# Optimization experiments

Hardware: AMD Instinct MI355X
Metric: run time of the kernel (lower is better)

The kernel has to match this reference:

```python
import jax, jax.numpy as jnp
import numpy as np

B, N, DIM = 4, 2048, 1024
HEADS, DH = 16, 64
INNER = HEADS * DH
SCALE = 8.0
EPS = 1e-5


def setup_inputs() -> dict:
    key = jax.random.key(0)
    ks = jax.random.split(key, 8)
    x = jax.random.normal(ks[0], (B, N, DIM), dtype=jnp.float32)
    context_mask = jax.random.bernoulli(ks[1], 0.9, (B, N))
    gamma = jnp.ones((DIM,), dtype=jnp.float32)
    null_kv = jax.random.normal(ks[2], (2, HEADS, 1, DH), dtype=jnp.float32)
    Wq = jax.random.normal(ks[3], (DIM, INNER), dtype=jnp.float32) * 0.02
    Wkv = jax.random.normal(ks[4], (DIM, 2 * INNER), dtype=jnp.float32) * 0.02
    # q_scale init: scale / dim_head**-0.5 = 8 * sqrt(64) = 64
    q_scale = jnp.full((DH,), SCALE * (DH ** 0.5), dtype=jnp.float32)
    k_scale = jnp.ones((DH,), dtype=jnp.float32)
    Wout = jax.random.normal(ks[5], (INNER, DIM), dtype=jnp.float32) * 0.02
    return {"x": x, "context_mask": context_mask, "gamma": gamma,
            "null_kv": null_kv, "Wq": Wq, "Wkv": Wkv,
            "q_scale": q_scale, "k_scale": k_scale, "Wout": Wout}


def _l2norm(t):
    return t / jnp.sqrt(jnp.sum(t * t, axis=-1, keepdims=True) + 1e-12)


def reference(x, context_mask, gamma, null_kv, Wq, Wkv, q_scale, k_scale, Wout):
    b, n, _ = x.shape
    # LayerNorm (beta buffer is zeros)
    mu = jnp.mean(x, axis=-1, keepdims=True)
    var = jnp.mean((x - mu) ** 2, axis=-1, keepdims=True)
    xn = (x - mu) / jnp.sqrt(var + EPS) * gamma
    # projections
    q = (xn @ Wq).reshape(b, n, HEADS, DH)
    kv = xn @ Wkv
    k = kv[..., :INNER].reshape(b, n, HEADS, DH)
    v = kv[..., INNER:].reshape(b, n, HEADS, DH)
    # null kv token: [h,1,d] -> [b,1,h,d]
    nk = jnp.broadcast_to(null_kv[0].transpose(1, 0, 2)[None], (b, 1, HEADS, DH))
    nv = jnp.broadcast_to(null_kv[1].transpose(1, 0, 2)[None], (b, 1, HEADS, DH))
    k = jnp.concatenate([nk, k], axis=1)  # [b, n+1, h, d]
    v = jnp.concatenate([nv, v], axis=1)
    # cosine-sim attention with learned per-dim scales
    q = _l2norm(q) * q_scale
    k = _l2norm(k) * k_scale
    # bias from mask (padded True for null token)
    mask = jnp.pad(context_mask, ((0, 0), (1, 0)), constant_values=True)
    bias = jnp.where(mask, 0.0, -10000.0)[:, None, None, :]  # [b,1,1,n+1]
    # memory_efficient_attention applies 1/sqrt(dh) internally
    scores = jnp.einsum('bqhd,bkhd->bhqk', q, k) * (DH ** -0.5) + bias
    attn = jax.nn.softmax(scores, axis=-1)
    out = jnp.einsum('bhqk,bkhd->bqhd', attn, v).reshape(b, n, INNER)
    return out @ Wout
```

## Files before the change

kernel.cpp:

```cpp
#include <hip/hip_runtime.h>
#include <hip/hip_bf16.h>
#include <stdint.h>


using f32x4  = __attribute__((ext_vector_type(4))) float;
using bf16x8 = __attribute__((ext_vector_type(8))) __bf16;
using f16x8  = __attribute__((ext_vector_type(8))) _Float16;
using uintv4 = __attribute__((ext_vector_type(4))) unsigned int;

__device__ __forceinline__ float b2f(unsigned short u) {
    return __uint_as_float(((unsigned)u) << 16);
}
__device__ __forceinline__ unsigned short f2b(float f) {
    unsigned u = __float_as_uint(f);
    u += 0x7fffu + ((u >> 16) & 1u);
    return (unsigned short)(u >> 16);
}
__device__ __forceinline__ unsigned short f2h(float f) {
    return __builtin_bit_cast(unsigned short, (_Float16)f);
}
__device__ __forceinline__ f32x4 mfma16(bf16x8 a, bf16x8 b, f32x4 c) {
    return __builtin_amdgcn_mfma_f32_16x16x32_bf16(a, b, c, 0, 0, 0);
}
__device__ __forceinline__ f32x4 mfma16h(f16x8 a, f16x8 b, f32x4 c) {
    return __builtin_amdgcn_mfma_f32_16x16x32_f16(a, b, c, 0, 0, 0);
}
__device__ __forceinline__ unsigned pk16(float a, float b) {
    return __builtin_bit_cast(unsigned, __builtin_amdgcn_cvt_pkrtz(a, b));
}
__device__ __forceinline__ void gl_lds16(const void* g, void* l) {
    __builtin_amdgcn_global_load_lds(
        (const __attribute__((address_space(1))) unsigned int*)g,
        (__attribute__((address_space(3))) unsigned int*)l, 16, 0, 0);
}

__global__ __launch_bounds__(256) void transpose_f2b(
    const float* __restrict__ in, unsigned short* __restrict__ out,
    int R, int C)
{
    __shared__ unsigned short t[32][33];
    int tx = threadIdx.x, ty = threadIdx.y;
    int c = blockIdx.x * 32 + tx;
#pragma unroll
    for (int i = 0; i < 4; ++i) {
        int r = blockIdx.y * 32 + ty + i * 8;
        t[ty + i * 8][tx] = f2b(in[(size_t)r * C + c]);
    }
    __syncthreads();
    int r2 = blockIdx.y * 32 + tx;
#pragma unroll
    for (int i = 0; i < 4; ++i) {
        int c2 = blockIdx.x * 32 + ty + i * 8;
        out[(size_t)c2 * R + r2] = t[tx][ty + i * 8];
    }
}

__global__ __launch_bounds__(256) void ln_kernel(
    const float* __restrict__ x, const float* __restrict__ gamma,
    unsigned short* __restrict__ xn)
{
    int row = blockIdx.x, tid = threadIdx.x;
    int wave = tid >> 6, lane = tid & 63;
    float4 raw = *(const float4*)(x + ((size_t)row << 10) + (tid << 2));
    float v[4] = { raw.x, raw.y, raw.z, raw.w };
    float s  = v[0] + v[1] + v[2] + v[3];
    float s2 = v[0]*v[0] + v[1]*v[1] + v[2]*v[2] + v[3]*v[3];
#pragma unroll
    for (int off = 1; off < 64; off <<= 1) {
        s  += __shfl_xor(s, off);
        s2 += __shfl_xor(s2, off);
    }
    __shared__ float ps[4], ps2[4], sh[2];
    if (lane == 0) { ps[wave] = s; ps2[wave] = s2; }
    __syncthreads();
    if (tid == 0) {
        float S  = ps[0] + ps[1] + ps[2] + ps[3];
        float S2 = ps2[0] + ps2[1] + ps2[2] + ps2[3];
        float mu  = S * (1.f / 1024.f);
        float var = S2 * (1.f / 1024.f) - mu * mu;
        sh[0] = mu; sh[1] = rsqrtf(var + 1e-5f);
    }
    __syncthreads();
    float mu = sh[0], rstd = sh[1];
    float4 g4 = *(const float4*)(gamma + (tid << 2));
    float g[4] = { g4.x, g4.y, g4.z, g4.w };
    unsigned short o[4];
#pragma unroll
    for (int i = 0; i < 4; ++i) o[i] = f2b((v[i] - mu) * rstd * g[i]);
    uint2 out;
    out.x = (unsigned)o[0] | ((unsigned)o[1] << 16);
    out.y = (unsigned)o[2] | ((unsigned)o[3] << 16);
    *(uint2*)(xn + ((size_t)row << 10) + (tid << 2)) = out;
}

template<int MODE>
__global__ __launch_bounds__(256, 2) void gemm_bt(
    const unsigned short* __restrict__ A, const unsigned short* __restrict__ Bt,
    void* __restrict__ Cout, const float* __restrict__ scale,
    unsigned short* __restrict__ Vout,
    int M, int N, int K, int ldc)
{
    __shared__ __bf16 As[128 * 32];
    __shared__ __bf16 Bs[128 * 32];
    int tid = threadIdx.x, lane = tid & 63, wave = tid >> 6;
    int quad = lane >> 4, l15 = lane & 15;
    int m0 = blockIdx.y * 128, n0 = blockIdx.x * 128;
    int wm = (wave & 1) * 64, wn = (wave >> 1) * 64;
    f32x4 acc[4][4] = {};

    const int srow = wave * 32 + (lane >> 2);
    const int scol = (lane & 3) << 3;
    const unsigned short* gA = A  + (size_t)(m0 + srow) * K + scol;
    const unsigned short* gB = Bt + (size_t)(n0 + srow) * K + scol;
    __bf16* lA0 = &As[(wave * 32) * 32];
    __bf16* lA1 = &As[(wave * 32 + 16) * 32];
    __bf16* lB0 = &Bs[(wave * 32) * 32];
    __bf16* lB1 = &Bs[(wave * 32 + 16) * 32];
    const size_t rstep = (size_t)16 * K;

    for (int k0 = 0; k0 < K; k0 += 32) {
        gl_lds16(gA,         lA0);
        gl_lds16(gA + rstep, lA1);
        gl_lds16(gB,         lB0);
        gl_lds16(gB + rstep, lB1);
        gA += 32; gB += 32;
        __syncthreads();
        bf16x8 af[4], bfv[4];
#pragma unroll
        for (int i = 0; i < 4; ++i)
            af[i] = *(const bf16x8*)&As[(wm + i * 16 + l15) * 32 + quad * 8];
#pragma unroll
        for (int j = 0; j < 4; ++j)
            bfv[j] = *(const bf16x8*)&Bs[(wn + j * 16 + l15) * 32 + quad * 8];
#pragma unroll
        for (int i = 0; i < 4; ++i)
#pragma unroll
            for (int j = 0; j < 4; ++j)
                acc[i][j] = mfma16(af[i], bfv[j], acc[i][j]);
        __syncthreads();
    }

    if (MODE == 2) {
#pragma unroll
        for (int i = 0; i < 4; ++i)
#pragma unroll
            for (int j = 0; j < 4; ++j) {
                int row = m0 + wm + i * 16 + quad * 4;
                int col = n0 + wn + j * 16 + l15;
                size_t base = (size_t)row * ldc + col;
#pragma unroll
                for (int r = 0; r < 4; ++r)
                    ((float*)Cout)[base + (size_t)r * ldc] = acc[i][j][r];
            }
        return;
    }

    if constexpr (MODE == 1) {
        const bool isv = (n0 + wn) >= 1024;
        if (isv) {
            __shared__ unsigned short Vx[4][64 * 64];
            unsigned short* tileL = Vx[wave];
            int hv = (n0 + wn - 1024) >> 6;
            int bidx = m0 >> 11;
            int tok0w = (m0 + wm) & 2047;
            size_t vbase = (size_t)((((bidx << 4) + hv) << 6)) * 2056;
#pragma unroll
            for (int i = 0; i < 4; ++i)
#pragma unroll
                for (int j = 0; j < 4; ++j) {
                    int d = j * 16 + l15;
                    int tk = (i * 16 + quad * 4) ^ ((d & 7) << 3);
                    unsigned u01 = (unsigned)f2h(acc[i][j][0])
                                 | ((unsigned)f2h(acc[i][j][1]) << 16);
                    unsigned u23 = (unsigned)f2h(acc[i][j][2])
                                 | ((unsigned)f2h(acc[i][j][3]) << 16);
                    *(unsigned*)&tileL[d * 64 + tk]     = u01;
                    *(unsigned*)&tileL[d * 64 + tk + 2] = u23;
                }
#pragma unroll
            for (int rr = 0; rr < 16; ++rr) {
                int d = rr * 4 + quad;
                uint2 val = *(const uint2*)
                    &tileL[d * 64 + ((l15 * 4) ^ ((d & 7) << 3))];
                *(uint2*)(Vout + vbase + (size_t)d * 2056 + tok0w + l15 * 4) = val;
            }
            return;
        }
    }

    float sc[4];
#pragma unroll
    for (int j = 0; j < 4; ++j) {
        float s = scale[j * 16 + l15];
        sc[j] = (MODE == 0) ? s * (0.125f * 1.44269504088896f) : s;
    }
#pragma unroll
    for (int i = 0; i < 4; ++i)
#pragma unroll
        for (int r = 0; r < 4; ++r) {
            float ss = 0.f;
#pragma unroll
            for (int j = 0; j < 4; ++j) ss += acc[i][j][r] * acc[i][j][r];
            ss += __shfl_xor(ss, 1); ss += __shfl_xor(ss, 2);
            ss += __shfl_xor(ss, 4); ss += __shfl_xor(ss, 8);
            float mul = rsqrtf(ss + 1e-12f);
            size_t rowbase = (size_t)(m0 + wm + i * 16 + quad * 4 + r) * ldc
                           + n0 + wn + l15;
#pragma unroll
            for (int j = 0; j < 4; ++j) {
                float v = acc[i][j][r];
                ((unsigned short*)Cout)[rowbase + j * 16] = f2b(v * mul * sc[j]);
            }
        }
}

__global__ __launch_bounds__(256) void nullkv_kernel(
    const float* __restrict__ null_kv, const float* __restrict__ k_scale,
    unsigned short* __restrict__ knull, unsigned short* __restrict__ Vt)
{
    int wave = threadIdx.x >> 6, lane = threadIdx.x & 63;
    int h = blockIdx.x * 4 + wave;
    int idx = (h << 6) + lane;
    float kvl = null_kv[idx];
    float ss = kvl * kvl;
#pragma unroll
    for (int off = 1; off < 64; off <<= 1) ss += __shfl_xor(ss, off);
    knull[idx] = f2b(kvl * rsqrtf(ss + 1e-12f) * k_scale[lane]);
    unsigned short vn = f2h(null_kv[1024 + idx]);
#pragma unroll
    for (int b = 0; b < 4; ++b)
        Vt[((size_t)(((b << 4) + h) << 6) + lane) * 2056 + 2048] = vn;
    int t = blockIdx.x * 256 + threadIdx.x;
#pragma unroll
    for (int rr = 0; rr < 4; ++rr) {
        size_t row = (size_t)t * 4 + rr;
#pragma unroll
        for (int c = 0; c < 7; ++c)
            Vt[row * 2056 + 2049 + c] = 0;
    }
}

__global__ __launch_bounds__(256, 4) void attn_kernel(
    const unsigned short* __restrict__ qn,
    const unsigned short* __restrict__ kvK,
    const unsigned short* __restrict__ knull,
    const unsigned short* __restrict__ Vt,
    const int* __restrict__ mask,
    unsigned short* __restrict__ ao)
{
    __shared__ __bf16    Kt[2][64 * 64];
    __shared__ _Float16  Vl[2][64 * 64];
    __shared__ __align__(16) float biasLds[2][64];

    const int tid = threadIdx.x, lane = tid & 63, wave = tid >> 6;
    const int quad = lane >> 4, l15 = lane & 15;
    const int bh = blockIdx.x;
    const int b = bh >> 4, h = bh & 15;
    const int mbase = blockIdx.y * 128 + wave * 32;
    const size_t rowoff = (size_t)b * 2048;

    bf16x8 qf[2][2];
#pragma unroll
    for (int rg = 0; rg < 2; ++rg)
#pragma unroll
        for (int ks = 0; ks < 2; ++ks)
            qf[rg][ks] = *(const bf16x8*)
                &qn[((rowoff + mbase + rg * 16 + l15) << 10) + (h << 6) + ks * 32 + quad * 8];

    const int t8  = lane >> 3;
    const int w7  = lane & 7;
    const int ksc = (w7 ^ t8) << 3;
    const size_t vrow0 = ((size_t)bh << 6);

    const int r0v = wave * 16 + t8;
    const int r1v = wave * 16 + 8 + t8;
    auto Tof = [](int r) {
        return ((r >> 5) << 5) | (((r >> 2) & 3) << 3)
             | (((r >> 4) & 1) << 2) | (r & 3);
    };
    const int T0 = Tof(r0v), T1 = Tof(r1v);

    const unsigned short* kp0 = kvK + ((rowoff + T0) << 10) + (h << 6) + ksc;
    const unsigned short* kp1 = kvK + ((rowoff + T1) << 10) + (h << 6) + ksc;
    const unsigned short* vp0 = Vt + (vrow0 + r0v) * 2056 + ((w7 ^ t8) << 3);
    const unsigned short* vp1 = Vt + (vrow0 + r1v) * 2056 + ((w7 ^ t8) << 3);

    auto issueFast = [&](int bf) {
        gl_lds16(kp0, &Kt[bf][(wave * 16) * 64]);
        gl_lds16(kp1, &Kt[bf][(wave * 16 + 8) * 64]);
        gl_lds16(vp0, &Vl[bf][(wave * 16) * 64]);
        gl_lds16(vp1, &Vl[bf][(wave * 16 + 8) * 64]);
        kp0 += 65536; kp1 += 65536;
        vp0 += 64; vp1 += 64;
    };
    auto issue32 = [&](int bf) {
        const unsigned short* kc =
            kvK + ((rowoff + 2047) << 10) + (h << 6) + ksc;
        const unsigned short* s0 = (T0 == 0) ? knull + (h << 6) + ksc : kc;
        gl_lds16(s0, &Kt[bf][(wave * 16) * 64]);
        gl_lds16(kc, &Kt[bf][(wave * 16 + 8) * 64]);
        gl_lds16(Vt + (vrow0 + r0v) * 2056 + 2048, &Vl[bf][(wave * 16) * 64]);
        gl_lds16(Vt + (vrow0 + r1v) * 2056 + 2048, &Vl[bf][(wave * 16 + 8) * 64]);
    };
    auto biasFor = [&](int nt) -> float {
        int j = (nt << 6) + lane;
        float bv = -512.f;
        if (j < 2048) { if (mask[(b << 11) + j] != 0) bv = 0.f; }
        else if (j == 2048) bv = 0.f;
        return bv;
    };

    const uintv4 onesu = { 0x3c003c00u, 0x3c003c00u, 0x3c003c00u, 0x3c003c00u };
    const f16x8 ones = __builtin_bit_cast(f16x8, onesu);

    f32x4 O[2][4] = {};
    f32x4 rsacc[2] = {};

    issueFast(0);
    float bcur = 0.f;
    if (wave == 0) bcur = biasFor(0);

    for (int nt = 0; nt < 33; ++nt) {
        const int buf = nt & 1;
        if (wave == 0) biasLds[buf][lane] = bcur;
        __syncthreads();
        if (nt < 31) {
            issueFast(buf ^ 1);
            if (wave == 0) bcur = biasFor(nt + 1);
        } else if (nt == 31) {
            issue32(buf ^ 1);
            if (wave == 0) bcur = biasFor(32);
        }

#pragma unroll
        for (int g = 0; g < 2; ++g) {
            float4 b0 = *(const float4*)&biasLds[buf][(g << 5) + (quad << 3)];
            float4 b1 = *(const float4*)&biasLds[buf][(g << 5) + (quad << 3) + 4];
            f32x4 s[2][2];
#pragma unroll
            for (int rg = 0; rg < 2; ++rg) {
                s[rg][0] = f32x4{ b0.x, b0.y, b0.z, b0.w };
                s[rg][1] = f32x4{ b1.x, b1.y, b1.z, b1.w };
            }
#pragma unroll
            for (int t = 0; t < 2; ++t) {
                const __bf16* kb = &Kt[buf][((g * 2 + t) * 16 + l15) * 64];
                bf16x8 k0 = *(const bf16x8*)&kb[(quad ^ (l15 & 7)) << 3];
                bf16x8 k1 = *(const bf16x8*)&kb[((4 + quad) ^ (l15 & 7)) << 3];
#pragma unroll
                for (int rg = 0; rg < 2; ++rg) {
                    s[rg][t] = mfma16(k0, qf[rg][0], s[rg][t]);
                    s[rg][t] = mfma16(k1, qf[rg][1], s[rg][t]);
                }
            }
            f16x8 vf8[4];
#pragma unroll
            for (int dt = 0; dt < 4; ++dt)
                vf8[dt] = *(const f16x8*)
                    &Vl[buf][(dt * 16 + l15) * 64
                             + ((((g << 2) + quad) ^ (l15 & 7)) << 3)];
#pragma unroll
            for (int rg = 0; rg < 2; ++rg) {
                float e0 = __builtin_amdgcn_exp2f(s[rg][0][0]);
                float e1 = __builtin_amdgcn_exp2f(s[rg][0][1]);
                float e2 = __builtin_amdgcn_exp2f(s[rg][0][2]);
                float e3 = __builtin_amdgcn_exp2f(s[rg][0][3]);
                float e4 = __builtin_amdgcn_exp2f(s[rg][1][0]);
                float e5 = __builtin_amdgcn_exp2f(s[rg][1][1]);
                float e6 = __builtin_amdgcn_exp2f(s[rg][1][2]);
                float e7 = __builtin_amdgcn_exp2f(s[rg][1][3]);
                uintv4 pu = { pk16(e0, e1), pk16(e2, e3),
                              pk16(e4, e5), pk16(e6, e7) };
                f16x8 p = __builtin_bit_cast(f16x8, pu);
                rsacc[rg] = mfma16h(p, ones, rsacc[rg]);
#pragma unroll
                for (int dt = 0; dt < 4; ++dt)
                    O[rg][dt] = mfma16h(p, vf8[dt], O[rg][dt]);
            }
        }
    }

#pragma unroll
    for (int rg = 0; rg < 2; ++rg) {
        float inv[4];
#pragma unroll
        for (int r = 0; r < 4; ++r) inv[r] = 1.f / rsacc[rg][r];
#pragma unroll
        for (int dt = 0; dt < 4; ++dt) {
            size_t base = ((rowoff + mbase + rg * 16 + quad * 4) << 10)
                        + (h << 6) + dt * 16 + l15;
#pragma unroll
            for (int r = 0; r < 4; ++r)
                ao[base + ((size_t)r << 10)] = f2b(O[rg][dt][r] * inv[r]);
        }
    }
}

extern "C" void kernel_launch(void* const* d_in, const int* in_sizes, int n_in,
                              void* d_out, int out_size, void* d_ws, size_t ws_size,
                              hipStream_t stream)
{
    const float* x       = (const float*)d_in[0];
    const int*   mask    = (const int*)d_in[1];
    const float* gamma   = (const float*)d_in[2];
    const float* null_kv = (const float*)d_in[3];
    const float* Wq      = (const float*)d_in[4];
    const float* Wkv     = (const float*)d_in[5];
    const float* q_scale = (const float*)d_in[6];
    const float* k_scale = (const float*)d_in[7];
    const float* Wout    = (const float*)d_in[8];

    char* ws = (char*)d_ws;
    const size_t VTG_OFF  = (size_t)48u << 20;
    const size_t VTG_SIZE = (size_t)4096 * 4112;
    unsigned short* xn    = (unsigned short*)(ws);
    unsigned short* ao    = xn;
    unsigned short* q     = (unsigned short*)(ws + ((size_t)16u << 20));
    unsigned short* kvK   = (unsigned short*)(ws + ((size_t)32u << 20));
    unsigned short* VtG   = (unsigned short*)(ws + VTG_OFF);
    unsigned short* WqT   = (unsigned short*)(ws + VTG_OFF + VTG_SIZE - ((size_t)2u << 20));
    unsigned short* WkvT  = (unsigned short*)(ws + VTG_OFF + VTG_SIZE);
    unsigned short* WoutT = (unsigned short*)(ws + VTG_OFF + VTG_SIZE + ((size_t)4u << 20));
    unsigned short* knull = (unsigned short*)(ws + VTG_OFF + VTG_SIZE + ((size_t)6u << 20));

    dim3 tb(32, 8);
    transpose_f2b<<<dim3(32, 32), tb, 0, stream>>>(Wq,   WqT,   1024, 1024);
    transpose_f2b<<<dim3(64, 32), tb, 0, stream>>>(Wkv,  WkvT,  1024, 2048);
    transpose_f2b<<<dim3(32, 32), tb, 0, stream>>>(Wout, WoutT, 1024, 1024);

    ln_kernel<<<8192, 256, 0, stream>>>(x, gamma, xn);

    gemm_bt<0><<<dim3(8, 64),  256, 0, stream>>>(xn, WqT, q, q_scale, nullptr,
                                                 8192, 1024, 1024, 1024);
    nullkv_kernel<<<4, 256, 0, stream>>>(null_kv, k_scale, knull, VtG);

    gemm_bt<1><<<dim3(16, 64), 256, 0, stream>>>(xn, WkvT, kvK, k_scale, VtG,
                                                 8192, 2048, 1024, 1024);

    attn_kernel<<<dim3(64, 16), 256, 0, stream>>>(q, kvK, knull, VtG, mask, ao);

    gemm_bt<2><<<dim3(8, 64), 256, 0, stream>>>(ao, WoutT, d_out, nullptr, nullptr,
                                                8192, 1024, 1024, 1024);
}
```

Baseline: 298.8 us.

## Fuse Q and KV projections into one GEMM with K=64 swizzled LDS tiles

Merges the Q and KV projection GEMMs into a single launch over a concatenated transposed weight (N=3072), routing each column block to the q, k or transposed-V outputs in the epilogue. The GEMM main loop now stages 64-wide K slices with an XOR swizzle in LDS, which halves the number of barriers per K and is meant to reduce bank conflicts. The Wout transpose is moved after attention and reuses the q buffer. Risk: the larger LDS footprint (32KB) may reduce occupancy, and the epilogue now branches per block.

New measurement: 289.5 us. -3.1%, faster.

```diff
diff --git a/kernel.cpp b/kernel.cpp
--- a/kernel.cpp
+++ b/kernel.cpp
@@ -8,9 +8,6 @@
 using f16x8  = __attribute__((ext_vector_type(8))) _Float16;
 using uintv4 = __attribute__((ext_vector_type(4))) unsigned int;
 
-__device__ __forceinline__ float b2f(unsigned short u) {
-    return __uint_as_float(((unsigned)u) << 16);
-}
 __device__ __forceinline__ unsigned short f2b(float f) {
     unsigned u = __float_as_uint(f);
     u += 0x7fffu + ((u >> 16) & 1u);
@@ -95,48 +92,62 @@
 
 template<int MODE>
 __global__ __launch_bounds__(256, 2) void gemm_bt(
-    const unsigned short* __restrict__ A, const unsigned short* __restrict__ Bt,
-    void* __restrict__ Cout, const float* __restrict__ scale,
+    const unsigned short* __restrict__ A,
+    const unsigned short* __restrict__ Bt,
+    void* __restrict__ C0,
+    unsigned short* __restrict__ Ck,
     unsigned short* __restrict__ Vout,
-    int M, int N, int K, int ldc)
-{
-    __shared__ __bf16 As[128 * 32];
-    __shared__ __bf16 Bs[128 * 32];
+    const float* __restrict__ qs, const float* __restrict__ ks,
+    int K)
+{
+    __shared__ __align__(16) unsigned char smem[32768];
+    __bf16* As = (__bf16*)smem;
+    __bf16* Bs = (__bf16*)(smem + 16384);
+
     int tid = threadIdx.x, lane = tid & 63, wave = tid >> 6;
     int quad = lane >> 4, l15 = lane & 15;
     int m0 = blockIdx.y * 128, n0 = blockIdx.x * 128;
     int wm = (wave & 1) * 64, wn = (wave >> 1) * 64;
     f32x4 acc[4][4] = {};
 
-    const int srow = wave * 32 + (lane >> 2);
-    const int scol = (lane & 3) << 3;
-    const unsigned short* gA = A  + (size_t)(m0 + srow) * K + scol;
-    const unsigned short* gB = Bt + (size_t)(n0 + srow) * K + scol;
-    __bf16* lA0 = &As[(wave * 32) * 32];
-    __bf16* lA1 = &As[(wave * 32 + 16) * 32];
-    __bf16* lB0 = &Bs[(wave * 32) * 32];
-    __bf16* lB1 = &Bs[(wave * 32 + 16) * 32];
-    const size_t rstep = (size_t)16 * K;
-
-    for (int k0 = 0; k0 < K; k0 += 32) {
-        gl_lds16(gA,         lA0);
-        gl_lds16(gA + rstep, lA1);
-        gl_lds16(gB,         lB0);
-        gl_lds16(gB + rstep, lB1);
-        gA += 32; gB += 32;
+    const int srow8 = lane >> 3;
+    const int w7    = lane & 7;
+    const int swz   = ((w7 ^ srow8) << 3);
+    const unsigned short* gA = A  + (size_t)(m0 + wave * 32 + srow8) * K + swz;
+    const unsigned short* gB = Bt + (size_t)(n0 + wave * 32 + srow8) * K + swz;
+    const size_t r8 = (size_t)8 * K;
+
+    const int nsteps = K >> 6;
+    for (int s = 0; s < nsteps; ++s) {
+#pragma unroll
+        for (int p = 0; p < 4; ++p)
+            gl_lds16(gA + p * r8, &As[(wave * 32 + p * 8) * 64]);
+#pragma unroll
+        for (int p = 0; p < 4; ++p)
+            gl_lds16(gB + p * r8, &Bs[(wave * 32 + p * 8) * 64]);
+        gA += 64; gB += 64;
         __syncthreads();
-        bf16x8 af[4], bfv[4];
-#pragma unroll
-        for (int i = 0; i < 4; ++i)
-            af[i] = *(const bf16x8*)&As[(wm + i * 16 + l15) * 32 + quad * 8];
-#pragma unroll
-        for (int j = 0; j < 4; ++j)
-            bfv[j] = *(const bf16x8*)&Bs[(wn + j * 16 + l15) * 32 + quad * 8];
-#pragma unroll
-        for (int i = 0; i < 4; ++i)
-#pragma unroll
-            for (int j = 0; j < 4; ++j)
-                acc[i][j] = mfma16(af[i], bfv[j], acc[i][j]);
+#pragma unroll
+        for (int kk = 0; kk < 2; ++kk) {
+            bf16x8 af[4], bfv[4];
+#pragma unroll
+            for (int i = 0; i < 4; ++i) {
+                int row = wm + i * 16 + l15;
+                int g = ((kk << 2) + quad) ^ (l15 & 7);
+                af[i] = *(const bf16x8*)&As[row * 64 + (g << 3)];
+            }
+#pragma unroll
+            for (int j = 0; j < 4; ++j) {
+                int row = wn + j * 16 + l15;
+                int g = ((kk << 2) + quad) ^ (l15 & 7);
+                bfv[j] = *(const bf16x8*)&Bs[row * 64 + (g << 3)];
+            }
+#pragma unroll
+            for (int i = 0; i < 4; ++i)
+#pragma unroll
+                for (int j = 0; j < 4; ++j)
+                    acc[i][j] = mfma16(af[i], bfv[j], acc[i][j]);
+        }
         __syncthreads();
     }
 
@@ -147,53 +158,52 @@
             for (int j = 0; j < 4; ++j) {
                 int row = m0 + wm + i * 16 + quad * 4;
                 int col = n0 + wn + j * 16 + l15;
-                size_t base = (size_t)row * ldc + col;
+                size_t base = (size_t)row * 1024 + col;
 #pragma unroll
                 for (int r = 0; r < 4; ++r)
-                    ((float*)Cout)[base + (size_t)r * ldc] = acc[i][j][r];
+                    ((float*)C0)[base + (size_t)r * 1024] = acc[i][j][r];
             }
         return;
     }
 
-    if constexpr (MODE == 1) {
-        const bool isv = (n0 + wn) >= 1024;
-        if (isv) {
-            __shared__ unsigned short Vx[4][64 * 64];
-            unsigned short* tileL = Vx[wave];
-            int hv = (n0 + wn - 1024) >> 6;
-            int bidx = m0 >> 11;
-            int tok0w = (m0 + wm) & 2047;
-            size_t vbase = (size_t)((((bidx << 4) + hv) << 6)) * 2056;
-#pragma unroll
-            for (int i = 0; i < 4; ++i)
-#pragma unroll
-                for (int j = 0; j < 4; ++j) {
-                    int d = j * 16 + l15;
-                    int tk = (i * 16 + quad * 4) ^ ((d & 7) << 3);
-                    unsigned u01 = (unsigned)f2h(acc[i][j][0])
-                                 | ((unsigned)f2h(acc[i][j][1]) << 16);
-                    unsigned u23 = (unsigned)f2h(acc[i][j][2])
-                                 | ((unsigned)f2h(acc[i][j][3]) << 16);
-                    *(unsigned*)&tileL[d * 64 + tk]     = u01;
-                    *(unsigned*)&tileL[d * 64 + tk + 2] = u23;
-                }
-#pragma unroll
-            for (int rr = 0; rr < 16; ++rr) {
-                int d = rr * 4 + quad;
-                uint2 val = *(const uint2*)
-                    &tileL[d * 64 + ((l15 * 4) ^ ((d & 7) << 3))];
-                *(uint2*)(Vout + vbase + (size_t)d * 2056 + tok0w + l15 * 4) = val;
-            }
-            return;
-        }
-    }
-
+    if (n0 >= 2048) {
+        unsigned short* tileL = (unsigned short*)smem + wave * 4096;
+        int hv = (n0 + wn - 2048) >> 6;
+        int bidx = m0 >> 11;
+        int tok0w = (m0 + wm) & 2047;
+        size_t vbase = (size_t)((((bidx << 4) + hv) << 6)) * 2056;
+#pragma unroll
+        for (int i = 0; i < 4; ++i)
+#pragma unroll
+            for (int j = 0; j < 4; ++j) {
+                int d = j * 16 + l15;
+                int tk = (i * 16 + quad * 4) ^ ((d & 7) << 3);
+                unsigned u01 = (unsigned)f2h(acc[i][j][0])
+                             | ((unsigned)f2h(acc[i][j][1]) << 16);
+                unsigned u23 = (unsigned)f2h(acc[i][j][2])
+                             | ((unsigned)f2h(acc[i][j][3]) << 16);
+                *(unsigned*)&tileL[d * 64 + tk]     = u01;
+                *(unsigned*)&tileL[d * 64 + tk + 2] = u23;
+            }
+#pragma unroll
+        for (int rr = 0; rr < 16; ++rr) {
+            int d = rr * 4 + quad;
+            uint2 val = *(const uint2*)
+                &tileL[d * 64 + ((l15 * 4) ^ ((d & 7) << 3))];
+            *(uint2*)(Vout + vbase + (size_t)d * 2056 + tok0w + l15 * 4) = val;
+        }
+        return;
+    }
+
+    const bool isQ = (n0 < 1024);
     float sc[4];
 #pragma unroll
     for (int j = 0; j < 4; ++j) {
-        float s = scale[j * 16 + l15];
-        sc[j] = (MODE == 0) ? s * (0.125f * 1.44269504088896f) : s;
-    }
+        float s = isQ ? qs[j * 16 + l15] : ks[j * 16 + l15];
+        sc[j] = isQ ? s * (0.125f * 1.44269504088896f) : s;
+    }
+    unsigned short* outp = isQ ? (unsigned short*)C0 : Ck;
+    const int coln0 = isQ ? n0 : (n0 - 1024);
 #pragma unroll
     for (int i = 0; i < 4; ++i)
 #pragma unroll
@@ -204,12 +214,12 @@
             ss += __shfl_xor(ss, 1); ss += __shfl_xor(ss, 2);
             ss += __shfl_xor(ss, 4); ss += __shfl_xor(ss, 8);
             float mul = rsqrtf(ss + 1e-12f);
-            size_t rowbase = (size_t)(m0 + wm + i * 16 + quad * 4 + r) * ldc
-                           + n0 + wn + l15;
+            size_t rowbase = (size_t)(m0 + wm + i * 16 + quad * 4 + r) * 1024
+                           + coln0 + wn + l15;
 #pragma unroll
             for (int j = 0; j < 4; ++j) {
                 float v = acc[i][j][r];
-                ((unsigned short*)Cout)[rowbase + j * 16] = f2b(v * mul * sc[j]);
+                outp[rowbase + j * 16] = f2b(v * mul * sc[j]);
             }
         }
 }
@@ -411,34 +421,34 @@
     const float* Wout    = (const float*)d_in[8];
 
     char* ws = (char*)d_ws;
-    const size_t VTG_OFF  = (size_t)48u << 20;
-    const size_t VTG_SIZE = (size_t)4096 * 4112;
+    const size_t VTG_OFF   = (size_t)48u << 20;
+    const size_t VTG_SIZE  = (size_t)4096 * 4112;
+    const size_t WQKV_OFF  = VTG_OFF + VTG_SIZE;
+    const size_t WQKV_SIZE = (size_t)3072 * 1024 * 2;
     unsigned short* xn    = (unsigned short*)(ws);
     unsigned short* ao    = xn;
     unsigned short* q     = (unsigned short*)(ws + ((size_t)16u << 20));
+    unsigned short* WoutT = q;
     unsigned short* kvK   = (unsigned short*)(ws + ((size_t)32u << 20));
     unsigned short* VtG   = (unsigned short*)(ws + VTG_OFF);
-    unsigned short* WqT   = (unsigned short*)(ws + VTG_OFF + VTG_SIZE - ((size_t)2u << 20));
-    unsigned short* WkvT  = (unsigned short*)(ws + VTG_OFF + VTG_SIZE);
-    unsigned short* WoutT = (unsigned short*)(ws + VTG_OFF + VTG_SIZE + ((size_t)4u << 20));
-    unsigned short* knull = (unsigned short*)(ws + VTG_OFF + VTG_SIZE + ((size_t)6u << 20));
+    unsigned short* WqkvT = (unsigned short*)(ws + WQKV_OFF);
+    unsigned short* knull = (unsigned short*)(ws + WQKV_OFF + WQKV_SIZE);
 
     dim3 tb(32, 8);
-    transpose_f2b<<<dim3(32, 32), tb, 0, stream>>>(Wq,   WqT,   1024, 1024);
-    transpose_f2b<<<dim3(64, 32), tb, 0, stream>>>(Wkv,  WkvT,  1024, 2048);
+    transpose_f2b<<<dim3(32, 32), tb, 0, stream>>>(Wq,  WqkvT,             1024, 1024);
+    transpose_f2b<<<dim3(64, 32), tb, 0, stream>>>(Wkv, WqkvT + (1u << 20), 1024, 2048);
+
+    ln_kernel<<<8192, 256, 0, stream>>>(x, gamma, xn);
+
+    nullkv_kernel<<<4, 256, 0, stream>>>(null_kv, k_scale, knull, VtG);
+
+    gemm_bt<0><<<dim3(24, 64), 256, 0, stream>>>(xn, WqkvT, q, kvK, VtG,
+                                                 q_scale, k_scale, 1024);
+
+    attn_kernel<<<dim3(64, 16), 256, 0, stream>>>(q, kvK, knull, VtG, mask, ao);
+
     transpose_f2b<<<dim3(32, 32), tb, 0, stream>>>(Wout, WoutT, 1024, 1024);
 
-    ln_kernel<<<8192, 256, 0, stream>>>(x, gamma, xn);
-
-    gemm_bt<0><<<dim3(8, 64),  256, 0, stream>>>(xn, WqT, q, q_scale, nullptr,
-                                                 8192, 1024, 1024, 1024);
-    nullkv_kernel<<<4, 256, 0, stream>>>(null_kv, k_scale, knull, VtG);
-
-    gemm_bt<1><<<dim3(16, 64), 256, 0, stream>>>(xn, WkvT, kvK, k_scale, VtG,
-                                                 8192, 2048, 1024, 1024);
-
-    attn_kernel<<<dim3(64, 16), 256, 0, stream>>>(q, kvK, knull, VtG, mask, ao);
-
     gemm_bt<2><<<dim3(8, 64), 256, 0, stream>>>(ao, WoutT, d_out, nullptr, nullptr,
-                                                8192, 1024, 1024, 1024);
-}
+                                                nullptr, nullptr, 1024);
+}
```
